# Kernel optimization log

Measured on AMD Instinct MI355X. Metric: run time of the kernel, lower is better.

The kernel has to match this reference:

```python
import jax, jax.numpy as jnp
import numpy as np

B, H, L = 256, 1024, 4
HQ, HKV, D = 16, 8, 64
I, V, C = 4096, 1027, 16
EPS = 1e-6
TEMP, TOP_P, TOP_K = 0.8, 0.6, 30
REP_PEN, REP_WIN = 1.1, 50


def _rms(x, w):
    return x * jax.lax.rsqrt(jnp.mean(x * x, axis=-1, keepdims=True) + EPS) * w


def _layer(h, wi, wq, wk, wv, qn, kn, wo, wp, wg, wu, wd):
    # h: [B,1,H]. seq_len == 1; RoPE at position 0 is identity (cos=1, sin=0).
    r = h
    x = _rms(h, wi)
    q = _rms((x @ wq).reshape(B, 1, HQ, D), qn)   # Qwen3 per-head q_norm
    k = _rms((x @ wk).reshape(B, 1, HKV, D), kn)  # Qwen3 per-head k_norm
    v = (x @ wv).reshape(B, 1, HKV, D)
    g = HQ // HKV
    kr = jnp.repeat(k, g, axis=2)
    vr = jnp.repeat(v, g, axis=2)
    s = jnp.einsum('bqhd,bkhd->bhqk', q, kr) / float(np.sqrt(D))
    a = jax.nn.softmax(s, axis=-1)
    o = jnp.einsum('bhqk,bkhd->bqhd', a, vr).reshape(B, 1, HQ * D) @ wo
    h = r + o
    r = h
    x = _rms(h, wp)
    m = (jax.nn.silu(x @ wg) * (x @ wu)) @ wd  # SwiGLU MLP
    return r + m


def _rep_penalty(scores, hist):
    # scores: [B,V], hist: [B,W] int token ids
    cur = jnp.take_along_axis(scores, hist, axis=1)
    new = jnp.where(cur < 0, cur * REP_PEN, cur / REP_PEN)
    return scores.at[jnp.arange(B)[:, None], hist].set(new)


def _sample(logits, key):
    l = logits / TEMP
    # top-k mask
    thr = jax.lax.top_k(l, TOP_K)[0][:, -1:]
    l = jnp.where(l < thr, -jnp.inf, l)
    # top-p: sort ascending, drop lowest-cumulative-prob <= 1 - top_p
    order = jnp.argsort(l, axis=-1)
    sl = jnp.take_along_axis(l, order, axis=1)
    cp = jnp.cumsum(jax.nn.softmax(sl, axis=-1), axis=-1)
    smask = cp <= 1.0 - TOP_P
    mask = jnp.zeros_like(l, dtype=bool).at[jnp.arange(B)[:, None], order].set(smask)
    l = jnp.where(mask, -jnp.inf, l)
    return jax.random.categorical(key, l, axis=-1)


def setup_inputs() -> dict:
    key = jax.random.key(0)
    ks = jax.random.split(key, 12)
    s = 0.02
    return {
        'backbone_hidden': jax.random.normal(ks[0], (B, 1, H), jnp.float32),
        'generated_history': jax.random.randint(ks[1], (B, 200, C), 0, V),
        'gen_step': 100,
        'embed_tables': jax.random.normal(ks[2], (C, V, H), jnp.float32) * s,
        'lm_heads': jax.random.normal(ks[3], (C, V, H), jnp.float32) * s,
        'w_in_norm': jnp.ones((L, H), jnp.float32),
        'w_q': jax.random.normal(ks[4], (L, H, HQ * D), jnp.float32) * s,
        'w_k': jax.random.normal(ks[5], (L, H, HKV * D), jnp.float32) * s,
        'w_v': jax.random.normal(ks[6], (L, H, HKV * D), jnp.float32) * s,
        'q_norm': jnp.ones((L, D), jnp.float32),
        'k_norm': jnp.ones((L, D), jnp.float32),
        'w_o': jax.random.normal(ks[7], (L, HQ * D, H), jnp.float32) * s,
        'w_post_norm': jnp.ones((L, H), jnp.float32),
        'w_gate': jax.random.normal(ks[8], (L, H, I), jnp.float32) * s,
        'w_up': jax.random.normal(ks[9], (L, H, I), jnp.float32) * s,
        'w_down': jax.random.normal(ks[10], (L, I, H), jnp.float32) * s,
        'final_norm': jnp.ones((H,), jnp.float32),
    }


def reference(backbone_hidden, generated_history, gen_step, embed_tables, lm_heads,
              w_in_norm, w_q, w_k, w_v, q_norm, k_norm, w_o, w_post_norm,
              w_gate, w_up, w_down, final_norm):
    keys = jax.random.split(jax.random.key(1234), C)
    hidden = backbone_hidden  # [B,1,H]
    toks = []
    for i in range(C):  # 16 sequential codebook steps
        h = hidden
        for l in range(L):  # 4 decoder layers
            h = _layer(h, w_in_norm[l], w_q[l], w_k[l], w_v[l], q_norm[l],
                       k_norm[l], w_o[l], w_post_norm[l], w_gate[l],
                       w_up[l], w_down[l])
        h = _rms(h, final_norm)
        logits = h[:, -1, :] @ lm_heads[i].T  # [B,V]
        hist = generated_history[:, :gen_step, i][:, -REP_WIN:]
        logits = _rep_penalty(logits, hist)
        tok = _sample(logits, keys[i])  # [B]
        toks.append(tok)
        if i < C - 1:
            hidden = embed_tables[i + 1][tok][:, None, :]  # [B,1,H]
    return jnp.stack(toks, axis=1)  # [B,C] int tokens
```

## Files before the change

kernel.cpp:

```cpp
#include <hip/hip_runtime.h>
#include <cstdint>
#include <cfloat>
#include <cmath>


#define PARTITIONABLE 1

namespace {
constexpr int B = 256, H = 1024, L = 4;
constexpr int I = 4096, V = 1027, C = 16;
constexpr int KV = 512;
}

__device__ __forceinline__ void tf2x32(uint32_t k0, uint32_t k1,
                                       uint32_t x0, uint32_t x1,
                                       uint32_t& o0, uint32_t& o1) {
  uint32_t k2 = k0 ^ k1 ^ 0x1BD11BDAu;
  x0 += k0; x1 += k1;
#define TFR(r) { x0 += x1; x1 = (x1 << r) | (x1 >> (32 - r)); x1 ^= x0; }
  TFR(13) TFR(15) TFR(26) TFR(6)
  x0 += k1; x1 += k2 + 1u;
  TFR(17) TFR(29) TFR(16) TFR(24)
  x0 += k2; x1 += k0 + 2u;
  TFR(13) TFR(15) TFR(26) TFR(6)
  x0 += k0; x1 += k1 + 3u;
  TFR(17) TFR(29) TFR(16) TFR(24)
  x0 += k1; x1 += k2 + 4u;
  TFR(13) TFR(15) TFR(26) TFR(6)
  x0 += k2; x1 += k0 + 5u;
#undef TFR
  o0 = x0; o1 = x1;
}

__device__ __forceinline__ float gumbel_for(uint32_t k0, uint32_t k1,
                                            uint32_t idx) {
  uint32_t o0, o1, bits;
  tf2x32(k0, k1, 0u, idx, o0, o1);
  bits = o0 ^ o1;
  float f = __uint_as_float((bits >> 9) | 0x3f800000u) - 1.0f;
  float u = fmaxf(FLT_MIN, f + FLT_MIN);
  return -logf(-logf(u));
}

__global__ __launch_bounds__(256) void copy_rms_k(const float* __restrict__ src,
                                                  float* __restrict__ h,
                                                  float* __restrict__ r) {
  int b = blockIdx.x, tid = threadIdx.x;
  float4 v = *(const float4*)&src[(size_t)b * H + tid * 4];
  *(float4*)&h[(size_t)b * H + tid * 4] = v;
  float s = v.x * v.x + v.y * v.y + v.z * v.z + v.w * v.w;
  for (int off = 32; off > 0; off >>= 1) s += __shfl_down(s, off, 64);
  __shared__ float red[4];
  if ((tid & 63) == 0) red[tid >> 6] = s;
  __syncthreads();
  if (tid == 0) {
    float t = red[0] + red[1] + red[2] + red[3];
    r[b] = 1.0f / sqrtf(t * (1.0f / 1024.0f) + 1e-6f);
  }
}

__global__ __launch_bounds__(256) void fold_k(const float* __restrict__ wo,
                                              float* __restrict__ wof) {
  int blk = blockIdx.x;
  int l = blk >> 9, c = blk & 511;
  int kb = c >> 6, jl = c & 63;
  const float* w = wo + (size_t)l * H * H;
  int k1 = kb * 128 + jl, k2 = k1 + 64;
  int j = threadIdx.x * 4;
  float4 a = *(const float4*)&w[(size_t)k1 * H + j];
  float4 bq = *(const float4*)&w[(size_t)k2 * H + j];
  float4 o = {a.x + bq.x, a.y + bq.y, a.z + bq.z, a.w + bq.w};
  *(float4*)&wof[((size_t)l * KV + c) * H + j] = o;
}

template <bool NORM, bool GATHER, bool BT, bool BOUND>
__global__ __launch_bounds__(256) void gemm64_k(
    const float* __restrict__ A, int lda,
    const float* __restrict__ rv, const float* __restrict__ wn,
    const float* __restrict__ Bm, int ldb,
    float* __restrict__ Cp, int N, int Kslice) {
  __shared__ __align__(16) float As[32][68];
  __shared__ __align__(16) float Bs[32][68];
  const int tid = threadIdx.x;
  const int tx = tid & 15, ty = tid >> 4;
  const int bm = blockIdx.y * 64;
  const int bn = blockIdx.x * 64;
  const int ks0 = blockIdx.z * Kslice;
  float4 acc[4];
#pragma unroll
  for (int i = 0; i < 4; ++i) acc[i] = float4{0.f, 0.f, 0.f, 0.f};

  for (int k0 = 0; k0 < Kslice; k0 += 32) {
    const int kbase = ks0 + k0;
#pragma unroll
    for (int s = 0; s < 2; ++s) {
      int slot = tid + s * 256;
      int rI = slot >> 3, c = slot & 7;
      int k = kbase + c * 4;
      int col = GATHER ? (((k >> 7) << 6) | (k & 63)) : k;
      float4 av = *(const float4*)&A[(size_t)(bm + rI) * lda + col];
      if (NORM) {
        float sc = rv[bm + rI];
        float4 wv = *(const float4*)&wn[k];
        av.x *= sc * wv.x; av.y *= sc * wv.y;
        av.z *= sc * wv.z; av.w *= sc * wv.w;
      }
      As[c * 4 + 0][rI] = av.x; As[c * 4 + 1][rI] = av.y;
      As[c * 4 + 2][rI] = av.z; As[c * 4 + 3][rI] = av.w;
    }
#pragma unroll
    for (int s = 0; s < 2; ++s) {
      int slot = tid + s * 256;
      if (!BT) {
        int kI = slot >> 4, c4 = slot & 15;
        float4 bv = *(const float4*)&Bm[(size_t)(kbase + kI) * ldb + bn + c4 * 4];
        *(float4*)&Bs[kI][c4 * 4] = bv;
      } else {
        int nI = slot >> 3, c = slot & 7;
        int n = bn + nI;
        float4 bv = {0.f, 0.f, 0.f, 0.f};
        if (!BOUND || n < N)
          bv = *(const float4*)&Bm[(size_t)n * ldb + kbase + c * 4];
        Bs[c * 4 + 0][nI] = bv.x; Bs[c * 4 + 1][nI] = bv.y;
        Bs[c * 4 + 2][nI] = bv.z; Bs[c * 4 + 3][nI] = bv.w;
      }
    }
    __syncthreads();
#pragma unroll
    for (int kk = 0; kk < 32; ++kk) {
      float4 a = *(const float4*)&As[kk][ty * 4];
      float4 b = *(const float4*)&Bs[kk][tx * 4];
      float ar[4] = {a.x, a.y, a.z, a.w};
#pragma unroll
      for (int i = 0; i < 4; ++i) {
        acc[i].x = fmaf(ar[i], b.x, acc[i].x);
        acc[i].y = fmaf(ar[i], b.y, acc[i].y);
        acc[i].z = fmaf(ar[i], b.z, acc[i].z);
        acc[i].w = fmaf(ar[i], b.w, acc[i].w);
      }
    }
    __syncthreads();
  }
  float* base = Cp + (size_t)blockIdx.z * 256 * N;
#pragma unroll
  for (int i = 0; i < 4; ++i) {
    int row = bm + ty * 4 + i;
    int colb = bn + tx * 4;
    if (!BOUND) {
      *(float4*)&base[(size_t)row * N + colb] = acc[i];
    } else {
      float vals[4] = {acc[i].x, acc[i].y, acc[i].z, acc[i].w};
      for (int j = 0; j < 4; ++j)
        if (colb + j < N) base[(size_t)row * N + colb + j] = vals[j];
    }
  }
}

__global__ __launch_bounds__(256) void gemm_gu_k(
    const float* __restrict__ hm, const float* __restrict__ rv,
    const float* __restrict__ wn,
    const float* __restrict__ Bg, const float* __restrict__ Bu,
    float* __restrict__ Mo) {
  __shared__ __align__(16) float As[32][68];
  __shared__ __align__(16) float Gs[32][36];
  __shared__ __align__(16) float Us[32][36];
  const int tid = threadIdx.x;
  const int tx = tid & 15, ty = tid >> 4;
  const int bm = blockIdx.y * 64;
  const int bn = blockIdx.x * 32;
  float2 ag[4], au[4];
#pragma unroll
  for (int i = 0; i < 4; ++i) { ag[i] = float2{0.f, 0.f}; au[i] = float2{0.f, 0.f}; }

  for (int k0 = 0; k0 < H; k0 += 32) {
#pragma unroll
    for (int s = 0; s < 2; ++s) {
      int slot = tid + s * 256;
      int rI = slot >> 3, c = slot & 7;
      int k = k0 + c * 4;
      float4 av = *(const float4*)&hm[(size_t)(bm + rI) * H + k];
      float sc = rv[bm + rI];
      float4 wv = *(const float4*)&wn[k];
      av.x *= sc * wv.x; av.y *= sc * wv.y;
      av.z *= sc * wv.z; av.w *= sc * wv.w;
      As[c * 4 + 0][rI] = av.x; As[c * 4 + 1][rI] = av.y;
      As[c * 4 + 2][rI] = av.z; As[c * 4 + 3][rI] = av.w;
    }
    {
      int kI = tid >> 3, c4 = tid & 7;
      float4 gv = *(const float4*)&Bg[(size_t)(k0 + kI) * I + bn + c4 * 4];
      float4 uv = *(const float4*)&Bu[(size_t)(k0 + kI) * I + bn + c4 * 4];
      *(float4*)&Gs[kI][c4 * 4] = gv;
      *(float4*)&Us[kI][c4 * 4] = uv;
    }
    __syncthreads();
#pragma unroll
    for (int kk = 0; kk < 32; ++kk) {
      float4 a = *(const float4*)&As[kk][ty * 4];
      float2 g = *(const float2*)&Gs[kk][tx * 2];
      float2 u = *(const float2*)&Us[kk][tx * 2];
      float ar[4] = {a.x, a.y, a.z, a.w};
#pragma unroll
      for (int i = 0; i < 4; ++i) {
        ag[i].x = fmaf(ar[i], g.x, ag[i].x);
        ag[i].y = fmaf(ar[i], g.y, ag[i].y);
        au[i].x = fmaf(ar[i], u.x, au[i].x);
        au[i].y = fmaf(ar[i], u.y, au[i].y);
      }
    }
    __syncthreads();
  }
#pragma unroll
  for (int i = 0; i < 4; ++i) {
    int row = bm + ty * 4 + i;
    int col = bn + tx * 2;
    float g0 = ag[i].x, g1 = ag[i].y;
    float s0 = 1.0f / (1.0f + expf(-g0));
    float s1 = 1.0f / (1.0f + expf(-g1));
    float2 o = {g0 * s0 * au[i].x, g1 * s1 * au[i].y};
    *(float2*)&Mo[(size_t)row * I + col] = o;
  }
}

__global__ __launch_bounds__(256) void red_v_k(const float* __restrict__ part,
                                               float* __restrict__ v, int S) {
  int i4 = (blockIdx.x * 256 + threadIdx.x) * 4;
  float4 s = {0.f, 0.f, 0.f, 0.f};
  for (int ss = 0; ss < S; ++ss) {
    float4 p = *(const float4*)&part[(size_t)ss * (256 * KV) + i4];
    s.x += p.x; s.y += p.y; s.z += p.z; s.w += p.w;
  }
  *(float4*)&v[i4] = s;
}

__global__ __launch_bounds__(256) void red_add_rms_k(const float* __restrict__ part,
                                                     float* __restrict__ h,
                                                     float* __restrict__ r, int S) {
  int b = blockIdx.x, tid = threadIdx.x;
  size_t off = (size_t)b * H + tid * 4;
  float4 a = *(const float4*)&h[off];
  for (int ss = 0; ss < S; ++ss) {
    float4 p = *(const float4*)&part[(size_t)ss * (256 * H) + off];
    a.x += p.x; a.y += p.y; a.z += p.z; a.w += p.w;
  }
  *(float4*)&h[off] = a;
  float s = a.x * a.x + a.y * a.y + a.z * a.z + a.w * a.w;
  for (int o = 32; o > 0; o >>= 1) s += __shfl_down(s, o, 64);
  __shared__ float red[4];
  if ((tid & 63) == 0) red[tid >> 6] = s;
  __syncthreads();
  if (tid == 0) {
    float t = red[0] + red[1] + red[2] + red[3];
    r[b] = 1.0f / sqrtf(t * (1.0f / 1024.0f) + 1e-6f);
  }
}

__global__ __launch_bounds__(256) void head_k(
    const float* __restrict__ part, int S,
    const int* __restrict__ gh, const int* __restrict__ gen_step_p,
    int step, const float* __restrict__ embed_next,
    float* __restrict__ h, float* __restrict__ r,
    int* __restrict__ out) {
  constexpr int TOPK = 30;
  constexpr int KMAX = 64;
  const int b = blockIdx.x, tid = threadIdx.x;
  __shared__ float sl[V];
  __shared__ float rv_[256]; __shared__ int ri[256];
  __shared__ float topv[TOPK]; __shared__ int topi[TOPK];
  __shared__ float kv[KMAX]; __shared__ int ki[KMAX]; __shared__ int keepf[KMAX];
  __shared__ uint32_t skey[2];
  __shared__ int scnt, sn, stok;
  __shared__ float redf[4];

  if (tid == 0) {
    uint32_t o0, o1;
    tf2x32(0u, 1234u, 0u, (uint32_t)step, o0, o1);
    skey[0] = o0; skey[1] = o1;
    scnt = 0;
  }
  for (int v = tid; v < V; v += 256) {
    float s = 0.f;
    for (int ss = 0; ss < S; ++ss)
      s += part[(size_t)ss * (256 * V) + (size_t)b * V + v];
    sl[v] = s;
  }
  __syncthreads();
  int gs = *gen_step_p;
  int cnt = gs < 50 ? gs : 50;
  int start = gs - cnt;
  int tkn = -1; float val = 0.f;
  if (tid < cnt) {
    tkn = gh[(size_t)b * 200 * C + (size_t)(start + tid) * C + step];
    val = sl[tkn];
  }
  __syncthreads();
  if (tid < cnt) sl[tkn] = (val < 0.f) ? val * 1.1f : val / 1.1f;
  __syncthreads();
  for (int v = tid; v < V; v += 256) sl[v] = sl[v] / 0.8f;
  __syncthreads();

  for (int it = 0; it < TOPK; ++it) {
    float bv = -INFINITY; int bi = 0x7fffffff;
    for (int v = tid; v < V; v += 256) {
      float x = sl[v];
      if (x > bv) { bv = x; bi = v; }
    }
    rv_[tid] = bv; ri[tid] = bi;
    __syncthreads();
    for (int s = 128; s > 0; s >>= 1) {
      if (tid < s) {
        float ov = rv_[tid + s]; int oi = ri[tid + s];
        if (ov > rv_[tid] || (ov == rv_[tid] && oi < ri[tid])) { rv_[tid] = ov; ri[tid] = oi; }
      }
      __syncthreads();
    }
    if (tid == 0) { topv[it] = rv_[0]; topi[it] = ri[0]; sl[ri[0]] = -INFINITY; }
    __syncthreads();
  }
  if (tid < TOPK) sl[topi[tid]] = topv[tid];
  __syncthreads();
  const float thr = topv[TOPK - 1];
  for (int v = tid; v < V; v += 256) {
    if (sl[v] >= thr) {
      int p = atomicAdd(&scnt, 1);
      if (p < KMAX) { kv[p] = sl[v]; ki[p] = v; }
    }
  }
  __syncthreads();

  if (tid == 0) {
    int n = scnt < KMAX ? scnt : KMAX;
    for (int a = 1; a < n; ++a) {
      float cv = kv[a]; int ci = ki[a];
      int p = a - 1;
      while (p >= 0 && (kv[p] > cv || (kv[p] == cv && ki[p] > ci))) {
        kv[p + 1] = kv[p]; ki[p + 1] = ki[p]; --p;
      }
      kv[p + 1] = cv; ki[p + 1] = ci;
    }
    float mx = kv[n - 1];
    float denom = 0.f;
    for (int j = 0; j < n; ++j) denom += expf(kv[j] - mx);
    float c = 0.f;
    for (int j = 0; j < n; ++j) {
      float p = expf(kv[j] - mx) / denom;
      c += p;
      keepf[j] = ((double)c > 0.4) ? 1 : 0;
    }
    sn = n;
  }
  __syncthreads();

  int n = sn;
  rv_[tid] = -INFINITY; ri[tid] = 0x7fffffff;
  if (tid < n && keepf[tid]) {
    uint32_t idx = (uint32_t)b * (uint32_t)V + (uint32_t)ki[tid];
    float g = gumbel_for(skey[0], skey[1], idx);
    rv_[tid] = kv[tid] + g;
    ri[tid] = ki[tid];
  }
  __syncthreads();
  for (int s = 128; s > 0; s >>= 1) {
    if (tid < s) {
      float ov = rv_[tid + s]; int oi = ri[tid + s];
      if (ov > rv_[tid] || (ov == rv_[tid] && oi < ri[tid])) { rv_[tid] = ov; ri[tid] = oi; }
    }
    __syncthreads();
  }
  if (tid == 0) {
    stok = ri[0];
    out[(size_t)b * C + step] = ri[0];
  }
  __syncthreads();

  if (embed_next != nullptr) {
    int tok = stok;
    float4 e = *(const float4*)&embed_next[(size_t)tok * H + tid * 4];
    *(float4*)&h[(size_t)b * H + tid * 4] = e;
    float s = e.x * e.x + e.y * e.y + e.z * e.z + e.w * e.w;
    for (int o = 32; o > 0; o >>= 1) s += __shfl_down(s, o, 64);
    if ((tid & 63) == 0) redf[tid >> 6] = s;
    __syncthreads();
    if (tid == 0) {
      float t = redf[0] + redf[1] + redf[2] + redf[3];
      r[b] = 1.0f / sqrtf(t * (1.0f / 1024.0f) + 1e-6f);
    }
  }
}

extern "C" void kernel_launch(void* const* d_in, const int* in_sizes, int n_in,
                              void* d_out, int out_size, void* d_ws, size_t ws_size,
                              hipStream_t stream) {
  const float* backbone = (const float*)d_in[0];
  const int*   gh       = (const int*)d_in[1];
  const int*   gen_step = (const int*)d_in[2];
  const float* embed    = (const float*)d_in[3];
  const float* lm       = (const float*)d_in[4];
  const float* w_in     = (const float*)d_in[5];
  const float* w_v      = (const float*)d_in[8];
  const float* w_o      = (const float*)d_in[11];
  const float* w_post   = (const float*)d_in[12];
  const float* w_g      = (const float*)d_in[13];
  const float* w_u      = (const float*)d_in[14];
  const float* w_d      = (const float*)d_in[15];
  const float* fnorm    = (const float*)d_in[16];
  int* out = (int*)d_out;
  float* ws = (float*)d_ws;

  const bool big = ws_size >= (size_t)22600000;
  float* h    = ws;
  float* v    = ws + 262144;
  float* m    = ws + 393216;
  float* wof  = big ? ws + 1441792 : nullptr;
  float* part = big ? ws + 3538944 : ws + 1441792;
  float* r    = big ? ws + 5642240 : ws + 1966080;

  const int S1 = big ? 16 : 4;
  const int S2 = big ? 8 : 2;
  const int S4 = big ? 8 : 2;
  const int S5 = big ? 8 : 1;

  copy_rms_k<<<dim3(256), dim3(256), 0, stream>>>(backbone, h, r);
  if (big) fold_k<<<dim3(2048), dim3(256), 0, stream>>>(w_o, wof);

  for (int i = 0; i < C; ++i) {
    for (int l = 0; l < L; ++l) {
      gemm64_k<true, false, false, false><<<dim3(8, 4, S1), dim3(256), 0, stream>>>(
          h, H, r, w_in + (size_t)l * H, w_v + (size_t)l * H * KV, KV,
          part, KV, H / S1);
      red_v_k<<<dim3(128), dim3(256), 0, stream>>>(part, v, S1);
      if (big)
        gemm64_k<false, false, false, false><<<dim3(16, 4, S2), dim3(256), 0, stream>>>(
            v, KV, nullptr, nullptr, wof + (size_t)l * KV * H, H,
            part, H, KV / S2);
      else
        gemm64_k<false, true, false, false><<<dim3(16, 4, S2), dim3(256), 0, stream>>>(
            v, KV, nullptr, nullptr, w_o + (size_t)l * H * H, H,
            part, H, H / S2);
      red_add_rms_k<<<dim3(256), dim3(256), 0, stream>>>(part, h, r, S2);
      gemm_gu_k<<<dim3(128, 4), dim3(256), 0, stream>>>(
          h, r, w_post + (size_t)l * H,
          w_g + (size_t)l * H * I, w_u + (size_t)l * H * I, m);
      gemm64_k<false, false, false, false><<<dim3(16, 4, S4), dim3(256), 0, stream>>>(
          m, I, nullptr, nullptr, w_d + (size_t)l * I * H, H,
          part, H, I / S4);
      red_add_rms_k<<<dim3(256), dim3(256), 0, stream>>>(part, h, r, S4);
    }
    gemm64_k<true, false, true, true><<<dim3(17, 4, S5), dim3(256), 0, stream>>>(
        h, H, r, fnorm, lm + (size_t)i * V * H, H, part, V, H / S5);
    head_k<<<dim3(256), dim3(256), 0, stream>>>(
        part, S5, gh, gen_step, i,
        (i < C - 1) ? embed + (size_t)(i + 1) * V * H : nullptr,
        h, r, out);
  }
}
```

Baseline: 11.29 ms.

## Emulate fp32 GEMMs with split-fp16 MFMA using pre-transposed split weights

Result: no change. 11.33 ms (+0.4%).

```diff
diff --git a/kernel.cpp b/kernel.cpp
--- a/kernel.cpp
+++ b/kernel.cpp
@@ -4,13 +4,16 @@
 #include <cmath>
 
 
-#define PARTITIONABLE 1
-
 namespace {
 constexpr int B = 256, H = 1024, L = 4;
 constexpr int I = 4096, V = 1027, C = 16;
 constexpr int KV = 512;
-}
+constexpr int VP = 1088;
+}
+
+typedef _Float16 half8_t __attribute__((ext_vector_type(8)));
+typedef _Float16 half4_t __attribute__((ext_vector_type(4)));
+typedef float f4_t __attribute__((ext_vector_type(4)));
 
 __device__ __forceinline__ void tf2x32(uint32_t k0, uint32_t k1,
                                        uint32_t x0, uint32_t x1,
@@ -34,29 +37,255 @@
 
 __device__ __forceinline__ float gumbel_for(uint32_t k0, uint32_t k1,
                                             uint32_t idx) {
-  uint32_t o0, o1, bits;
+  uint32_t o0, o1;
   tf2x32(k0, k1, 0u, idx, o0, o1);
-  bits = o0 ^ o1;
+  uint32_t bits = o0 ^ o1;
   float f = __uint_as_float((bits >> 9) | 0x3f800000u) - 1.0f;
   float u = fmaxf(FLT_MIN, f + FLT_MIN);
   return -logf(-logf(u));
 }
 
-__global__ __launch_bounds__(256) void copy_rms_k(const float* __restrict__ src,
-                                                  float* __restrict__ h,
-                                                  float* __restrict__ r) {
+__device__ __forceinline__ void split1(float x, _Float16& hi, _Float16& lo) {
+  _Float16 h = (_Float16)x;
+  float d = x - (float)h;
+  hi = h;
+  lo = (_Float16)(d * 2048.0f);
+}
+
+template <bool FOLD>
+__global__ __launch_bounds__(256) void split_t_k(
+    const float* __restrict__ W, _Float16* __restrict__ Wh,
+    _Float16* __restrict__ Wl, int Kout, int Nin,
+    size_t in_stride, size_t out_stride) {
+  __shared__ float ts[32][33];
+  const float* w = W + blockIdx.z * in_stride;
+  _Float16* oh = Wh + blockIdx.z * out_stride;
+  _Float16* ol = Wl + blockIdx.z * out_stride;
+  const int n0 = blockIdx.x * 32, k0 = blockIdx.y * 32;
+  const int tid = threadIdx.x;
+  {
+    int r = tid >> 3, c4 = (tid & 7) * 4;
+    int kk = k0 + r;
+    float4 v;
+    if (FOLD) {
+      int k1 = ((kk >> 6) << 7) + (kk & 63);
+      float4 a = *(const float4*)&w[(size_t)k1 * Nin + n0 + c4];
+      float4 b = *(const float4*)&w[(size_t)(k1 + 64) * Nin + n0 + c4];
+      v = float4{a.x + b.x, a.y + b.y, a.z + b.z, a.w + b.w};
+    } else {
+      v = *(const float4*)&w[(size_t)kk * Nin + n0 + c4];
+    }
+    ts[r][c4 + 0] = v.x; ts[r][c4 + 1] = v.y;
+    ts[r][c4 + 2] = v.z; ts[r][c4 + 3] = v.w;
+  }
+  __syncthreads();
+  {
+    int n = tid >> 3, kc = (tid & 7) * 4;
+    half4_t hh, ll;
+#pragma unroll
+    for (int j = 0; j < 4; ++j) {
+      _Float16 a, b;
+      split1(ts[kc + j][n], a, b);
+      hh[j] = a; ll[j] = b;
+    }
+    size_t off = (size_t)(n0 + n) * Kout + k0 + kc;
+    *(half4_t*)&oh[off] = hh;
+    *(half4_t*)&ol[off] = ll;
+  }
+}
+
+__global__ __launch_bounds__(256) void split_lm_k(
+    const float* __restrict__ lm, _Float16* __restrict__ Lh,
+    _Float16* __restrict__ Ll) {
+  size_t flat = ((size_t)blockIdx.x * 256 + threadIdx.x) * 4;
+  if (flat >= (size_t)C * VP * H) return;
+  int i = (int)(flat / ((size_t)VP * H));
+  size_t rem = flat - (size_t)i * VP * H;
+  int n = (int)(rem / H);
+  int k = (int)(rem - (size_t)n * H);
+  float4 v = {0.f, 0.f, 0.f, 0.f};
+  if (n < V) v = *(const float4*)&lm[(size_t)i * V * H + (size_t)n * H + k];
+  half4_t hh, ll;
+  float xs[4] = {v.x, v.y, v.z, v.w};
+#pragma unroll
+  for (int j = 0; j < 4; ++j) { _Float16 a, b; split1(xs[j], a, b); hh[j] = a; ll[j] = b; }
+  *(half4_t*)&Lh[flat] = hh;
+  *(half4_t*)&Ll[flat] = ll;
+}
+
+__global__ __launch_bounds__(256) void copy_rms_split_k(
+    const float* __restrict__ src, float* __restrict__ h, float* __restrict__ r,
+    const float* __restrict__ wn, _Float16* __restrict__ xh,
+    _Float16* __restrict__ xl) {
   int b = blockIdx.x, tid = threadIdx.x;
   float4 v = *(const float4*)&src[(size_t)b * H + tid * 4];
   *(float4*)&h[(size_t)b * H + tid * 4] = v;
   float s = v.x * v.x + v.y * v.y + v.z * v.z + v.w * v.w;
-  for (int off = 32; off > 0; off >>= 1) s += __shfl_down(s, off, 64);
+  for (int o = 32; o > 0; o >>= 1) s += __shfl_down(s, o, 64);
   __shared__ float red[4];
+  __shared__ float sr;
   if ((tid & 63) == 0) red[tid >> 6] = s;
   __syncthreads();
   if (tid == 0) {
     float t = red[0] + red[1] + red[2] + red[3];
-    r[b] = 1.0f / sqrtf(t * (1.0f / 1024.0f) + 1e-6f);
-  }
+    sr = 1.0f / sqrtf(t * (1.0f / 1024.0f) + 1e-6f);
+    r[b] = sr;
+  }
+  __syncthreads();
+  if (xh) {
+    float rr = sr;
+    float4 w = *(const float4*)&wn[tid * 4];
+    float xs[4] = {v.x * rr * w.x, v.y * rr * w.y, v.z * rr * w.z, v.w * rr * w.w};
+    half4_t hh, ll;
+#pragma unroll
+    for (int j = 0; j < 4; ++j) { _Float16 a, c; split1(xs[j], a, c); hh[j] = a; ll[j] = c; }
+    *(half4_t*)&xh[(size_t)b * H + tid * 4] = hh;
+    *(half4_t*)&xl[(size_t)b * H + tid * 4] = ll;
+  }
+}
+
+__global__ __launch_bounds__(256) void red_v_split_k(
+    const float* __restrict__ part, int S,
+    _Float16* __restrict__ vh, _Float16* __restrict__ vl) {
+  int i4 = (blockIdx.x * 256 + threadIdx.x) * 4;
+  float4 s = {0.f, 0.f, 0.f, 0.f};
+  for (int ss = 0; ss < S; ++ss) {
+    float4 p = *(const float4*)&part[(size_t)ss * (256 * KV) + i4];
+    s.x += p.x; s.y += p.y; s.z += p.z; s.w += p.w;
+  }
+  half4_t hh, ll;
+  float xs[4] = {s.x, s.y, s.z, s.w};
+#pragma unroll
+  for (int j = 0; j < 4; ++j) { _Float16 a, b; split1(xs[j], a, b); hh[j] = a; ll[j] = b; }
+  *(half4_t*)&vh[i4] = hh;
+  *(half4_t*)&vl[i4] = ll;
+}
+
+__global__ __launch_bounds__(256) void red_add_rms_split_k(
+    const float* __restrict__ part, int S, float* __restrict__ h,
+    float* __restrict__ r, const float* __restrict__ wn,
+    _Float16* __restrict__ xh, _Float16* __restrict__ xl) {
+  int b = blockIdx.x, tid = threadIdx.x;
+  size_t off = (size_t)b * H + tid * 4;
+  float4 a = *(const float4*)&h[off];
+  for (int ss = 0; ss < S; ++ss) {
+    float4 p = *(const float4*)&part[(size_t)ss * (256 * H) + off];
+    a.x += p.x; a.y += p.y; a.z += p.z; a.w += p.w;
+  }
+  *(float4*)&h[off] = a;
+  float s = a.x * a.x + a.y * a.y + a.z * a.z + a.w * a.w;
+  for (int o = 32; o > 0; o >>= 1) s += __shfl_down(s, o, 64);
+  __shared__ float red[4];
+  __shared__ float sr;
+  if ((tid & 63) == 0) red[tid >> 6] = s;
+  __syncthreads();
+  if (tid == 0) {
+    float t = red[0] + red[1] + red[2] + red[3];
+    sr = 1.0f / sqrtf(t * (1.0f / 1024.0f) + 1e-6f);
+    r[b] = sr;
+  }
+  __syncthreads();
+  if (xh) {
+    float rr = sr;
+    float4 w = *(const float4*)&wn[tid * 4];
+    float xs[4] = {a.x * rr * w.x, a.y * rr * w.y, a.z * rr * w.z, a.w * rr * w.w};
+    half4_t hh, ll;
+#pragma unroll
+    for (int j = 0; j < 4; ++j) { _Float16 p, q; split1(xs[j], p, q); hh[j] = p; ll[j] = q; }
+    *(half4_t*)&xh[off] = hh;
+    *(half4_t*)&xl[off] = ll;
+  }
+}
+
+__global__ __launch_bounds__(256) void red_gu_split_k(
+    const float* __restrict__ Pg, const float* __restrict__ Pu, int S,
+    _Float16* __restrict__ mh, _Float16* __restrict__ ml) {
+  int i4 = (blockIdx.x * 256 + threadIdx.x) * 4;
+  float4 g = {0.f, 0.f, 0.f, 0.f}, u = {0.f, 0.f, 0.f, 0.f};
+  for (int ss = 0; ss < S; ++ss) {
+    float4 pg = *(const float4*)&Pg[(size_t)ss * (256 * I) + i4];
+    float4 pu = *(const float4*)&Pu[(size_t)ss * (256 * I) + i4];
+    g.x += pg.x; g.y += pg.y; g.z += pg.z; g.w += pg.w;
+    u.x += pu.x; u.y += pu.y; u.z += pu.z; u.w += pu.w;
+  }
+  float gs[4] = {g.x, g.y, g.z, g.w};
+  float us[4] = {u.x, u.y, u.z, u.w};
+  half4_t hh, ll;
+#pragma unroll
+  for (int j = 0; j < 4; ++j) {
+    float sg = 1.0f / (1.0f + expf(-gs[j]));
+    float m = gs[j] * sg * us[j];
+    _Float16 a, b; split1(m, a, b); hh[j] = a; ll[j] = b;
+  }
+  *(half4_t*)&mh[i4] = hh;
+  *(half4_t*)&ml[i4] = ll;
+}
+
+template <bool TWO_B>
+__global__ __launch_bounds__(256) void mgemm_k(
+    const _Float16* __restrict__ Ah, const _Float16* __restrict__ Al,
+    const _Float16* __restrict__ Bh0, const _Float16* __restrict__ Bl0,
+    const _Float16* __restrict__ B2h, const _Float16* __restrict__ B2l,
+    float* __restrict__ P0, float* __restrict__ P2,
+    int K, int Kslice, int ldp, int nb) {
+  int bx = blockIdx.x;
+  const _Float16* Bh = Bh0;
+  const _Float16* Bl = Bl0;
+  float* out = P0;
+  if (TWO_B && bx >= nb) { bx -= nb; Bh = B2h; Bl = B2l; out = P2; }
+  const int tid = threadIdx.x, lane = tid & 63, wv = tid >> 6;
+  const int wm = (wv & 1) * 32, wn = (wv >> 1) * 32;
+  const int l15 = lane & 15, quad = lane >> 4;
+  const int mrow = blockIdx.y * 128 + wm + l15;
+  const int nrow = bx * 64 + wn + l15;
+  const int ks0 = blockIdx.z * Kslice;
+  f4_t c1[2][2][2] = {};
+  f4_t c2[2][2][2] = {};
+  for (int k0 = ks0; k0 < ks0 + Kslice; k0 += 32) {
+    const int kq = k0 + quad * 8;
+    half8_t bh[2], bl[2];
+#pragma unroll
+    for (int g = 0; g < 2; ++g) {
+      size_t ro = (size_t)(nrow + g * 16) * K + kq;
+      bh[g] = *(const half8_t*)&Bh[ro];
+      bl[g] = *(const half8_t*)&Bl[ro];
+    }
+#pragma unroll
+    for (int mt = 0; mt < 2; ++mt) {
+      half8_t ah[2], al[2];
+#pragma unroll
+      for (int g = 0; g < 2; ++g) {
+        size_t ro = (size_t)(mrow + mt * 64 + g * 16) * K + kq;
+        ah[g] = *(const half8_t*)&Ah[ro];
+        al[g] = *(const half8_t*)&Al[ro];
+      }
+#pragma unroll
+      for (int gi = 0; gi < 2; ++gi)
+#pragma unroll
+        for (int gj = 0; gj < 2; ++gj) {
+          c1[mt][gi][gj] = __builtin_amdgcn_mfma_f32_16x16x32_f16(
+              ah[gi], bh[gj], c1[mt][gi][gj], 0, 0, 0);
+          c2[mt][gi][gj] = __builtin_amdgcn_mfma_f32_16x16x32_f16(
+              ah[gi], bl[gj], c2[mt][gi][gj], 0, 0, 0);
+          c2[mt][gi][gj] = __builtin_amdgcn_mfma_f32_16x16x32_f16(
+              al[gi], bh[gj], c2[mt][gi][gj], 0, 0, 0);
+        }
+    }
+  }
+  float* base = out + (size_t)blockIdx.z * 256 * ldp;
+#pragma unroll
+  for (int mt = 0; mt < 2; ++mt)
+#pragma unroll
+    for (int gi = 0; gi < 2; ++gi)
+#pragma unroll
+      for (int gj = 0; gj < 2; ++gj)
+#pragma unroll
+        for (int i = 0; i < 4; ++i) {
+          int row = blockIdx.y * 128 + mt * 64 + wm + gi * 16 + quad * 4 + i;
+          int col = bx * 64 + wn + gj * 16 + l15;
+          base[(size_t)row * ldp + col] =
+              c1[mt][gi][gj][i] + c2[mt][gi][gj][i] * (1.0f / 2048.0f);
+        }
 }
 
 __global__ __launch_bounds__(256) void fold_k(const float* __restrict__ wo,
@@ -144,8 +373,7 @@
   float* base = Cp + (size_t)blockIdx.z * 256 * N;
 #pragma unroll
   for (int i = 0; i < 4; ++i) {
-    int row = bm + ty * 4 + i;
-    int colb = bn + tx * 4;
+    int row = bm + ty * 4 + i, colb = bn + tx * 4;
     if (!BOUND) {
       *(float4*)&base[(size_t)row * N + colb] = acc[i];
     } else {
@@ -171,7 +399,6 @@
   float2 ag[4], au[4];
 #pragma unroll
   for (int i = 0; i < 4; ++i) { ag[i] = float2{0.f, 0.f}; au[i] = float2{0.f, 0.f}; }
-
   for (int k0 = 0; k0 < H; k0 += 32) {
 #pragma unroll
     for (int s = 0; s < 2; ++s) {
@@ -212,8 +439,7 @@
   }
 #pragma unroll
   for (int i = 0; i < 4; ++i) {
-    int row = bm + ty * 4 + i;
-    int col = bn + tx * 2;
+    int row = bm + ty * 4 + i, col = bn + tx * 2;
     float g0 = ag[i].x, g1 = ag[i].y;
     float s0 = 1.0f / (1.0f + expf(-g0));
     float s1 = 1.0f / (1.0f + expf(-g1));
@@ -256,11 +482,12 @@
 }
 
 __global__ __launch_bounds__(256) void head_k(
-    const float* __restrict__ part, int S,
+    const float* __restrict__ part, int S, int ldp,
     const int* __restrict__ gh, const int* __restrict__ gen_step_p,
     int step, const float* __restrict__ embed_next,
     float* __restrict__ h, float* __restrict__ r,
-    int* __restrict__ out) {
+    const float* __restrict__ win0, _Float16* __restrict__ xh,
+    _Float16* __restrict__ xl, int* __restrict__ out) {
   constexpr int TOPK = 30;
   constexpr int KMAX = 64;
   const int b = blockIdx.x, tid = threadIdx.x;
@@ -271,6 +498,7 @@
   __shared__ uint32_t skey[2];
   __shared__ int scnt, sn, stok;
   __shared__ float redf[4];
+  __shared__ float srr;
 
   if (tid == 0) {
     uint32_t o0, o1;
@@ -281,7 +509,7 @@
   for (int v = tid; v < V; v += 256) {
     float s = 0.f;
     for (int ss = 0; ss < S; ++ss)
-      s += part[(size_t)ss * (256 * V) + (size_t)b * V + v];
+      s += part[(size_t)ss * 256 * ldp + (size_t)b * ldp + v];
     sl[v] = s;
   }
   __syncthreads();
@@ -383,7 +611,19 @@
     __syncthreads();
     if (tid == 0) {
       float t = redf[0] + redf[1] + redf[2] + redf[3];
-      r[b] = 1.0f / sqrtf(t * (1.0f / 1024.0f) + 1e-6f);
+      srr = 1.0f / sqrtf(t * (1.0f / 1024.0f) + 1e-6f);
+      r[b] = srr;
+    }
+    __syncthreads();
+    if (xh) {
+      float rr = srr;
+      float4 w = *(const float4*)&win0[tid * 4];
+      float xs[4] = {e.x * rr * w.x, e.y * rr * w.y, e.z * rr * w.z, e.w * rr * w.w};
+      half4_t hh, ll;
+#pragma unroll
+      for (int j = 0; j < 4; ++j) { _Float16 p, q; split1(xs[j], p, q); hh[j] = p; ll[j] = q; }
+      *(half4_t*)&xh[(size_t)b * H + tid * 4] = hh;
+      *(half4_t*)&xl[(size_t)b * H + tid * 4] = ll;
     }
   }
 }
@@ -405,9 +645,100 @@
   const float* w_d      = (const float*)d_in[15];
   const float* fnorm    = (const float*)d_in[16];
   int* out = (int*)d_out;
+
+  const size_t NEED_A = 329253888ull;
+  const size_t NEED_B = 257950720ull;
+  int tier = (ws_size >= NEED_A) ? 0 : (ws_size >= NEED_B) ? 1
+           : (ws_size >= 22600000ull) ? 2 : 3;
+
+  if (tier <= 1) {
+    uint8_t* wsb = (uint8_t*)d_ws;
+    float*     h    = (float*)(wsb + 0);
+    float*     r    = (float*)(wsb + 1048576);
+    _Float16*  Asp  = (_Float16*)(wsb + 1049600);
+    float*     P    = (float*)(wsb + 5243904);
+    float*     P2   = (float*)(wsb + 23069696);
+    _Float16*  wvh  = (_Float16*)(wsb + 39846912);
+    _Float16*  woh  = (_Float16*)(wsb + 48235520);
+    _Float16*  wgh  = (_Float16*)(wsb + 56624128);
+    _Float16*  wuh  = (_Float16*)(wsb + 123732992);
+    _Float16*  wdh  = (_Float16*)(wsb + 190841856);
+    _Float16*  lmh  = (_Float16*)(wsb + 257950720);
+    _Float16*  wvl = wvh + (size_t)L * KV * H;
+    _Float16*  wol = woh + (size_t)L * H * KV;
+    _Float16*  wgl = wgh + (size_t)L * I * H;
+    _Float16*  wul = wuh + (size_t)L * I * H;
+    _Float16*  wdl = wdh + (size_t)L * H * I;
+    _Float16*  lml = lmh + (size_t)C * VP * H;
+
+    split_t_k<false><<<dim3(KV / 32, H / 32, L), dim3(256), 0, stream>>>(
+        w_v, wvh, wvl, H, KV, (size_t)H * KV, (size_t)KV * H);
+    split_t_k<true><<<dim3(H / 32, KV / 32, L), dim3(256), 0, stream>>>(
+        w_o, woh, wol, KV, H, (size_t)H * H, (size_t)H * KV);
+    split_t_k<false><<<dim3(I / 32, H / 32, L), dim3(256), 0, stream>>>(
+        w_g, wgh, wgl, H, I, (size_t)H * I, (size_t)I * H);
+    split_t_k<false><<<dim3(I / 32, H / 32, L), dim3(256), 0, stream>>>(
+        w_u, wuh, wul, H, I, (size_t)H * I, (size_t)I * H);
+    split_t_k<false><<<dim3(H / 32, I / 32, L), dim3(256), 0, stream>>>(
+        w_d, wdh, wdl, I, H, (size_t)I * H, (size_t)H * I);
+    if (tier == 0) {
+      int nthr = (C * VP * H) / 4;
+      split_lm_k<<<dim3((nthr + 255) / 256), dim3(256), 0, stream>>>(lm, lmh, lml);
+    }
+
+    _Float16* xh = Asp;                 _Float16* xl = Asp + 256 * H;
+    _Float16* vh = Asp;                 _Float16* vl = Asp + 256 * KV;
+    _Float16* mh = Asp;                 _Float16* ml = Asp + 256 * I;
+
+    copy_rms_split_k<<<dim3(256), dim3(256), 0, stream>>>(
+        backbone, h, r, w_in, xh, xl);
+
+    constexpr int S1 = 8, S2 = 8, S3 = 4, S4 = 16, S5 = 8;
+    for (int i = 0; i < C; ++i) {
+      for (int l = 0; l < L; ++l) {
+        mgemm_k<false><<<dim3(8, 2, S1), dim3(256), 0, stream>>>(
+            xh, xl, wvh + (size_t)l * KV * H, wvl + (size_t)l * KV * H,
+            nullptr, nullptr, P, nullptr, H, H / S1, KV, 8);
+        red_v_split_k<<<dim3(128), dim3(256), 0, stream>>>(P, S1, vh, vl);
+        mgemm_k<false><<<dim3(16, 2, S2), dim3(256), 0, stream>>>(
+            vh, vl, woh + (size_t)l * H * KV, wol + (size_t)l * H * KV,
+            nullptr, nullptr, P, nullptr, KV, KV / S2, H, 16);
+        red_add_rms_split_k<<<dim3(256), dim3(256), 0, stream>>>(
+            P, S2, h, r, w_post + (size_t)l * H, xh, xl);
+        mgemm_k<true><<<dim3(128, 2, S3), dim3(256), 0, stream>>>(
+            xh, xl, wgh + (size_t)l * I * H, wgl + (size_t)l * I * H,
+            wuh + (size_t)l * I * H, wul + (size_t)l * I * H,
+            P, P2, H, H / S3, I, 64);
+        red_gu_split_k<<<dim3(1024), dim3(256), 0, stream>>>(P, P2, S3, mh, ml);
+        mgemm_k<false><<<dim3(16, 2, S4), dim3(256), 0, stream>>>(
+            mh, ml, wdh + (size_t)l * H * I, wdl + (size_t)l * H * I,
+            nullptr, nullptr, P, nullptr, I, I / S4, H, 16);
+        red_add_rms_split_k<<<dim3(256), dim3(256), 0, stream>>>(
+            P, S4, h, r, (l < L - 1) ? w_in + (size_t)(l + 1) * H : fnorm,
+            xh, xl);
+      }
+      int ldp;
+      int S5eff;
+      if (tier == 0) {
+        mgemm_k<false><<<dim3(17, 2, S5), dim3(256), 0, stream>>>(
+            xh, xl, lmh + (size_t)i * VP * H, lml + (size_t)i * VP * H,
+            nullptr, nullptr, P, nullptr, H, H / S5, VP, 17);
+        ldp = VP; S5eff = S5;
+      } else {
+        gemm64_k<true, false, true, true><<<dim3(17, 4, 8), dim3(256), 0, stream>>>(
+            h, H, r, fnorm, lm + (size_t)i * V * H, H, P, V, H / 8);
+        ldp = V; S5eff = 8;
+      }
+      head_k<<<dim3(256), dim3(256), 0, stream>>>(
+          P, S5eff, ldp, gh, gen_step, i,
+          (i < C - 1) ? embed + (size_t)(i + 1) * V * H : nullptr,
+          h, r, w_in, xh, xl, out);
+    }
+    return;
+  }
+
   float* ws = (float*)d_ws;
-
-  const bool big = ws_size >= (size_t)22600000;
+  const bool big = (tier == 2);
   float* h    = ws;
   float* v    = ws + 262144;
   float* m    = ws + 393216;
@@ -420,7 +751,8 @@
   const int S4 = big ? 8 : 2;
   const int S5 = big ? 8 : 1;
 
-  copy_rms_k<<<dim3(256), dim3(256), 0, stream>>>(backbone, h, r);
+  copy_rms_split_k<<<dim3(256), dim3(256), 0, stream>>>(
+      backbone, h, r, nullptr, nullptr, nullptr);
   if (big) fold_k<<<dim3(2048), dim3(256), 0, stream>>>(w_o, wof);
 
   for (int i = 0; i < C; ++i) {
@@ -449,8 +781,8 @@
     gemm64_k<true, false, true, true><<<dim3(17, 4, S5), dim3(256), 0, stream>>>(
         h, H, r, fnorm, lm + (size_t)i * V * H, H, part, V, H / S5);
     head_k<<<dim3(256), dim3(256), 0, stream>>>(
-        part, S5, gh, gen_step, i,
+        part, S5, V, gh, gen_step, i,
         (i < C - 1) ? embed + (size_t)(i + 1) * V * H : nullptr,
-        h, r, out);
-  }
-}
+        h, r, nullptr, nullptr, nullptr, out);
+  }
+}
```
